# Performance work log

Hardware: AMD Instinct MI355X
Metric: run time of the kernel (lower is better)

Reference implementation:

```python
import jax, jax.numpy as jnp
import numpy as np

EPS = 1e-8

def setup_inputs() -> dict:
    key = jax.random.key(0)
    k1, k2, k3, k4, k5 = jax.random.split(key, 5)
    B, S, d, H = 4, 1024, 512, 8
    hd = d // H
    x = jax.random.normal(k1, (B, S, d), dtype=jnp.float32)
    V = jax.random.normal(k2, (B, S, H, hd), dtype=jnp.float32)
    # binary biological mask [B, S, S]
    M = (jax.random.uniform(k3, (B, S, S)) > 0.5).astype(jnp.float32)
    in_proj_w = jax.random.normal(k4, (3 * d, d), dtype=jnp.float32) * 0.02
    in_proj_b = jnp.zeros((3 * d,), dtype=jnp.float32)
    out_w = jax.random.normal(k5, (d, d), dtype=jnp.float32) * 0.02
    out_b = jnp.zeros((d,), dtype=jnp.float32)
    return {"x": x, "V": V, "M": M, "in_proj_w": in_proj_w,
            "in_proj_b": in_proj_b, "out_w": out_w, "out_b": out_b}


def reference(x, V, M, in_proj_w, in_proj_b, out_w, out_b):
    B, S, d = x.shape
    H, hd = V.shape[2], V.shape[3]
    # packed QKV projection (torch MHA in_proj); V slice is computed by torch
    # but its result is discarded, so only Q,K slices influence the output.
    qkv = x @ in_proj_w.T + in_proj_b            # [B, S, 3d]
    q = qkv[..., :d].reshape(B, S, H, hd).transpose(0, 2, 1, 3)        # [B,H,S,hd]
    k = qkv[..., d:2 * d].reshape(B, S, H, hd).transpose(0, 2, 1, 3)   # [B,H,S,hd]
    scores = jnp.einsum("bhqd,bhkd->bhqk", q, k) / jnp.sqrt(jnp.float32(hd))
    A = jax.nn.softmax(scores, axis=-1)           # [B,H,S,S] per-head attn weights
    # biological mask + L1 renormalization (post-hoc, as in original)
    A_sparse = A * M[:, None, :, :]
    norm = jnp.sum(jnp.abs(A_sparse), axis=-1, keepdims=True) + EPS
    A_bar = A_sparse / norm
    # custom V: [B,S,H,hd] -> [B,H,S,hd]
    Vp = V.transpose(0, 2, 1, 3)
    out = jnp.einsum("bhqk,bhkd->bhqd", A_bar, Vp)  # [B,H,S,hd]
    out = out.transpose(0, 2, 1, 3).reshape(B, S, d)
    return out @ out_w.T + out_b
```

## Files before the change

kernel.cpp:

```cpp
#include <hip/hip_runtime.h>
#include <hip/hip_bf16.h>

#define BB 4
#define SS 1024
#define DD 512
#define HH 8
#define HD 64

typedef __attribute__((ext_vector_type(8))) short bf16x8;
typedef __attribute__((ext_vector_type(4))) float f32x4;

static __device__ __forceinline__ unsigned short f2b(float f) {
  union { float f; unsigned int u; } c; c.f = f;
  return (unsigned short)((c.u + 0x7fffu + ((c.u >> 16) & 1u)) >> 16);
}

__global__ __launch_bounds__(256) void prep(
    const float* __restrict__ x, const float* __restrict__ W1,
    const float* __restrict__ Wo, const float* __restrict__ Mmask,
    const float* __restrict__ V, unsigned short* __restrict__ xb,
    unsigned short* __restrict__ W1b, unsigned short* __restrict__ Wob,
    unsigned char* __restrict__ Mpack, unsigned short* __restrict__ Vt) {
  __shared__ float Ls[64][65];
  const int bid = blockIdx.x;
  const int tid = threadIdx.x;

  if (bid < 1408) {
    const float* src; unsigned short* dst; size_t off;
    if (bid < 1024) { src = x;  dst = xb;  off = ((size_t)bid * 256 + tid) * 8; }
    else if (bid < 1280) { src = W1; dst = W1b; off = ((size_t)(bid - 1024) * 256 + tid) * 8; }
    else { src = Wo; dst = Wob; off = ((size_t)(bid - 1280) * 256 + tid) * 8; }
    const float4 a = *(const float4*)(src + off);
    const float4 b = *(const float4*)(src + off + 4);
    union { unsigned short s[8]; uint4 v; } o;
    o.s[0] = f2b(a.x); o.s[1] = f2b(a.y); o.s[2] = f2b(a.z); o.s[3] = f2b(a.w);
    o.s[4] = f2b(b.x); o.s[5] = f2b(b.y); o.s[6] = f2b(b.z); o.s[7] = f2b(b.w);
    *(uint4*)(dst + off) = o.v;
  } else if (bid < 3456) {
    const size_t g = (size_t)(bid - 1408) * 256 + tid;
    const float4 a = *(const float4*)(Mmask + g * 8);
    const float4 b = *(const float4*)(Mmask + g * 8 + 4);
    unsigned v = 0;
    v |= (a.x > 0.5f) ? 1u : 0u;   v |= (a.y > 0.5f) ? 2u : 0u;
    v |= (a.z > 0.5f) ? 4u : 0u;   v |= (a.w > 0.5f) ? 8u : 0u;
    v |= (b.x > 0.5f) ? 16u : 0u;  v |= (b.y > 0.5f) ? 32u : 0u;
    v |= (b.z > 0.5f) ? 64u : 0u;  v |= (b.w > 0.5f) ? 128u : 0u;
    Mpack[g] = (unsigned char)v;
  } else {
    const int id = bid - 3456;
    const int s0 = (id & 15) * 64, h = (id >> 4) & 7, b = id >> 7;
    {
      const int r = tid >> 2, cs = (tid & 3) * 16;
      const float* src = V + ((size_t)((b * SS + s0 + r) * HH) + h) * HD + cs;
#pragma unroll
      for (int j = 0; j < 4; j++) {
        const float4 v = *(const float4*)(src + j * 4);
        Ls[r][cs + j * 4 + 0] = v.x; Ls[r][cs + j * 4 + 1] = v.y;
        Ls[r][cs + j * 4 + 2] = v.z; Ls[r][cs + j * 4 + 3] = v.w;
      }
    }
    __syncthreads();
    {
      const int d = tid >> 2, ss = (tid & 3) * 16;
      union { unsigned short s[16]; uint4 v[2]; } o;
#pragma unroll
      for (int j = 0; j < 16; j++) o.s[j] = f2b(Ls[ss + j][d]);
      unsigned short* dst =
          Vt + ((size_t)((b * HH + h) * HD + d)) * SS + s0 + ss;
      *(uint4*)dst = o.v[0];
      *(uint4*)(dst + 8) = o.v[1];
    }
  }
}

__global__ __launch_bounds__(256) void gemm_qk(
    const unsigned short* __restrict__ xb, const unsigned short* __restrict__ W1b,
    const float* __restrict__ bias, unsigned short* __restrict__ qkb) {
  __shared__ unsigned short As[128][40];
  __shared__ unsigned short Bs[64][40];
  const int tid = threadIdx.x;
  const int lane = tid & 63, wave = tid >> 6;
  const int l16 = lane & 15, quad = lane >> 4;
  const int row0 = blockIdx.y * 128, col0 = blockIdx.x * 64;

  f32x4 acc[2][4];
#pragma unroll
  for (int i = 0; i < 2; i++)
#pragma unroll
    for (int j = 0; j < 4; j++) acc[i][j] = (f32x4){0.f, 0.f, 0.f, 0.f};

  for (int k0 = 0; k0 < DD; k0 += 32) {
    __syncthreads();
    {
      const int r = tid >> 1, cs = (tid & 1) * 16;
      const unsigned short* s = xb + (size_t)(row0 + r) * DD + k0 + cs;
      *(uint4*)&As[r][cs] = *(const uint4*)s;
      *(uint4*)&As[r][cs + 8] = *(const uint4*)(s + 8);
    }
    {
      const int r = tid >> 2, cs = (tid & 3) * 8;
      *(uint4*)&Bs[r][cs] =
          *(const uint4*)(W1b + (size_t)(col0 + r) * DD + k0 + cs);
    }
    __syncthreads();

    const bf16x8 a0 = *(const bf16x8*)&As[wave * 32 + l16][quad * 8];
    const bf16x8 a1 = *(const bf16x8*)&As[wave * 32 + 16 + l16][quad * 8];
#pragma unroll
    for (int nt = 0; nt < 4; nt++) {
      const bf16x8 bb = *(const bf16x8*)&Bs[nt * 16 + l16][quad * 8];
      acc[0][nt] = __builtin_amdgcn_mfma_f32_16x16x32_bf16(a0, bb, acc[0][nt], 0, 0, 0);
      acc[1][nt] = __builtin_amdgcn_mfma_f32_16x16x32_bf16(a1, bb, acc[1][nt], 0, 0, 0);
    }
  }

#pragma unroll
  for (int nt = 0; nt < 4; nt++) {
    const int col = col0 + nt * 16 + l16;
    const float bv = bias[col];
#pragma unroll
    for (int mi = 0; mi < 2; mi++)
#pragma unroll
      for (int reg = 0; reg < 4; reg++) {
        const int row = row0 + wave * 32 + mi * 16 + quad * 4 + reg;
        qkb[(size_t)row * 1024 + col] = f2b(acc[mi][nt][reg] + bv);
      }
  }
}

__global__ __launch_bounds__(256) void gemm_out(
    const unsigned short* __restrict__ Ab, const unsigned short* __restrict__ Wob,
    const float* __restrict__ bias, float* __restrict__ out) {
  __shared__ unsigned short As[64][40];
  __shared__ unsigned short Bs[64][40];
  const int tid = threadIdx.x;
  const int lane = tid & 63, wave = tid >> 6;
  const int l16 = lane & 15, quad = lane >> 4;
  const int row0 = blockIdx.y * 64, col0 = blockIdx.x * 64;

  f32x4 acc[4];
#pragma unroll
  for (int j = 0; j < 4; j++) acc[j] = (f32x4){0.f, 0.f, 0.f, 0.f};

  for (int k0 = 0; k0 < DD; k0 += 32) {
    __syncthreads();
    {
      const int r = tid >> 2, cs = (tid & 3) * 8;
      *(uint4*)&As[r][cs] =
          *(const uint4*)(Ab + (size_t)(row0 + r) * DD + k0 + cs);
      *(uint4*)&Bs[r][cs] =
          *(const uint4*)(Wob + (size_t)(col0 + r) * DD + k0 + cs);
    }
    __syncthreads();

    const bf16x8 a0 = *(const bf16x8*)&As[wave * 16 + l16][quad * 8];
#pragma unroll
    for (int nt = 0; nt < 4; nt++) {
      const bf16x8 bb = *(const bf16x8*)&Bs[nt * 16 + l16][quad * 8];
      acc[nt] = __builtin_amdgcn_mfma_f32_16x16x32_bf16(a0, bb, acc[nt], 0, 0, 0);
    }
  }

#pragma unroll
  for (int nt = 0; nt < 4; nt++) {
    const int col = col0 + nt * 16 + l16;
    const float bv = bias[col];
#pragma unroll
    for (int reg = 0; reg < 4; reg++) {
      const int row = row0 + wave * 16 + quad * 4 + reg;
      out[(size_t)row * DD + col] = acc[nt][reg] + bv;
    }
  }
}

__global__ __launch_bounds__(256) void flash_attn_split(
    const unsigned short* __restrict__ qkb, const unsigned short* __restrict__ Vt,
    const unsigned char* __restrict__ Mpack, float* __restrict__ Opart,
    float* __restrict__ Sms) {
  __shared__ unsigned short QP[64][72];
  __shared__ unsigned short Ks[64][72];
  __shared__ unsigned short Vs[64][72];

  const int tid = threadIdx.x;
  const int lane = tid & 63, wave = tid >> 6;
  const int l16 = lane & 15, quad = lane >> 4;
  const int q0 = blockIdx.x * 64;
  const int h = blockIdx.y & 7, sp = blockIdx.y >> 3;
  const int b = blockIdx.z;

  {
    const int r = tid >> 2, cs = (tid & 3) * 16;
    const unsigned short* s = qkb + (size_t)(b * SS + q0 + r) * 1024 + h * HD + cs;
    *(uint4*)&QP[r][cs] = *(const uint4*)s;
    *(uint4*)&QP[r][cs + 8] = *(const uint4*)(s + 8);
  }

  union { uint4 v[4]; unsigned w[16]; } mu;
  {
    const uint4* mp = (const uint4*)(Mpack +
        (size_t)(b * SS + q0 + wave * 16 + l16) * 128 + sp * 64);
    mu.v[0] = mp[0]; mu.v[1] = mp[1]; mu.v[2] = mp[2]; mu.v[3] = mp[3];
  }

  __syncthreads();
  const bf16x8 bQ0 = *(const bf16x8*)&QP[wave * 16 + l16][quad * 8];
  const bf16x8 bQ1 = *(const bf16x8*)&QP[wave * 16 + l16][32 + quad * 8];
  unsigned short(*Ps)[72] = (unsigned short(*)[72]) & QP[wave * 16][0];

  float Smp = 0.f;
  f32x4 O[4];
#pragma unroll
  for (int i = 0; i < 4; i++) O[i] = (f32x4){0.f, 0.f, 0.f, 0.f};

#pragma unroll
  for (int i = 0; i < 8; i++) {
    const int k0 = (sp * 8 + i) * 64;
    const unsigned mlo = mu.w[2 * i], mhi = mu.w[2 * i + 1];

    __syncthreads();
    {
      const int r = tid >> 2, cs = (tid & 3) * 16;
      const unsigned short* s =
          qkb + (size_t)(b * SS + k0 + r) * 1024 + DD + h * HD + cs;
      *(uint4*)&Ks[r][cs] = *(const uint4*)s;
      *(uint4*)&Ks[r][cs + 8] = *(const uint4*)(s + 8);
    }
    {
      const int d = tid >> 2, cs = (tid & 3) * 16;
      const unsigned short* s =
          Vt + ((size_t)((b * HH + h) * HD + d)) * SS + k0 + cs;
      *(uint4*)&Vs[d][cs] = *(const uint4*)s;
      *(uint4*)&Vs[d][cs + 8] = *(const uint4*)(s + 8);
    }
    __syncthreads();

#pragma unroll
    for (int t = 0; t < 4; t++) {
      const bf16x8 aK0 = *(const bf16x8*)&Ks[t * 16 + l16][quad * 8];
      const bf16x8 aK1 = *(const bf16x8*)&Ks[t * 16 + l16][32 + quad * 8];
      f32x4 a = (f32x4){0.f, 0.f, 0.f, 0.f};
      a = __builtin_amdgcn_mfma_f32_16x16x32_bf16(aK0, bQ0, a, 0, 0, 0);
      a = __builtin_amdgcn_mfma_f32_16x16x32_bf16(aK1, bQ1, a, 0, 0, 0);
      const unsigned nib =
          ((t < 2 ? mlo : mhi) >> ((t & 1) * 16 + quad * 4)) & 0xFu;
      float e0 = __expf(a[0] * 0.125f); e0 = (nib & 1u) ? e0 : 0.f;
      float e1 = __expf(a[1] * 0.125f); e1 = (nib & 2u) ? e1 : 0.f;
      float e2 = __expf(a[2] * 0.125f); e2 = (nib & 4u) ? e2 : 0.f;
      float e3 = __expf(a[3] * 0.125f); e3 = (nib & 8u) ? e3 : 0.f;
      Smp += (e0 + e1) + (e2 + e3);
      uint2 w;
      w.x = (unsigned)f2b(e0) | ((unsigned)f2b(e1) << 16);
      w.y = (unsigned)f2b(e2) | ((unsigned)f2b(e3) << 16);
      *(uint2*)&Ps[l16][t * 16 + quad * 4] = w;
    }

    const bf16x8 aP0 = *(const bf16x8*)&Ps[l16][quad * 8];
    const bf16x8 aP1 = *(const bf16x8*)&Ps[l16][32 + quad * 8];
#pragma unroll
    for (int dt = 0; dt < 4; dt++) {
      const bf16x8 bV0 = *(const bf16x8*)&Vs[dt * 16 + l16][quad * 8];
      const bf16x8 bV1 = *(const bf16x8*)&Vs[dt * 16 + l16][32 + quad * 8];
      O[dt] = __builtin_amdgcn_mfma_f32_16x16x32_bf16(aP0, bV0, O[dt], 0, 0, 0);
      O[dt] = __builtin_amdgcn_mfma_f32_16x16x32_bf16(aP1, bV1, O[dt], 0, 0, 0);
    }
  }

  Smp += __shfl_xor(Smp, 16);
  Smp += __shfl_xor(Smp, 32);
  const size_t grow0 = (size_t)(b * HH + h) * SS + q0 + wave * 16;
  const int NR = BB * HH * SS;
  if (lane < 16) Sms[(size_t)sp * NR + grow0 + lane] = Smp;
#pragma unroll
  for (int reg = 0; reg < 4; reg++) {
    const size_t obase = ((size_t)sp * NR + grow0 + quad * 4 + reg) * HD;
#pragma unroll
    for (int dt = 0; dt < 4; dt++)
      Opart[obase + dt * 16 + l16] = O[dt][reg];
  }
}

__global__ __launch_bounds__(256) void combine(
    const float* __restrict__ Opart, const float* __restrict__ Sms,
    unsigned short* __restrict__ attnb) {
  const int idx = blockIdx.x * 256 + threadIdx.x;
  const int row = idx >> 4;
  const int d = (idx & 15) * 4;
  const int NR = BB * HH * SS;
  const float4 o0 = *(const float4*)(Opart + (size_t)row * HD + d);
  const float4 o1 = *(const float4*)(Opart + ((size_t)NR + row) * HD + d);
  const float s = Sms[row] + Sms[NR + row];
  const float inv = 1.0f / (s + 1e-12f);
  const int b = row >> 13, h = (row >> 10) & 7, q = row & 1023;
  union { unsigned short us[4]; uint2 v; } o;
  o.us[0] = f2b((o0.x + o1.x) * inv);
  o.us[1] = f2b((o0.y + o1.y) * inv);
  o.us[2] = f2b((o0.z + o1.z) * inv);
  o.us[3] = f2b((o0.w + o1.w) * inv);
  *(uint2*)(attnb + (size_t)(b * SS + q) * DD + h * HD + d) = o.v;
}

extern "C" void kernel_launch(void* const* d_in, const int* in_sizes, int n_in,
                              void* d_out, int out_size, void* d_ws,
                              size_t ws_size, hipStream_t stream) {
  const float* x = (const float*)d_in[0];
  const float* V = (const float*)d_in[1];
  const float* Mmask = (const float*)d_in[2];
  const float* in_proj_w = (const float*)d_in[3];
  const float* in_proj_b = (const float*)d_in[4];
  const float* out_w = (const float*)d_in[5];
  const float* out_b = (const float*)d_in[6];
  float* out = (float*)d_out;

  unsigned char* ws = (unsigned char*)d_ws;
  unsigned short* qkb   = (unsigned short*)(ws);
  unsigned short* xb    = (unsigned short*)(ws + (8ull << 20));
  unsigned short* W1b   = (unsigned short*)(ws + (12ull << 20));
  unsigned short* Wob   = (unsigned short*)(ws + (13ull << 20));
  unsigned short* Vt    = (unsigned short*)(ws + (14ull << 20));
  unsigned short* attnb = (unsigned short*)(ws + (18ull << 20));
  float*          Opart = (float*)(ws + (22ull << 20));
  float*          Sms   = (float*)(ws + (38ull << 20));
  unsigned char*  Mpack = ws + (38ull << 20) + (256u << 10);

  prep<<<3968, 256, 0, stream>>>(x, in_proj_w, out_w, Mmask, V,
                                 xb, W1b, Wob, Mpack, Vt);
  gemm_qk<<<dim3(16, 32), 256, 0, stream>>>(xb, W1b, in_proj_b, qkb);
  flash_attn_split<<<dim3(SS / 64, 2 * HH, BB), 256, 0, stream>>>(
      qkb, Vt, Mpack, Opart, Sms);
  combine<<<2048, 256, 0, stream>>>(Opart, Sms, attnb);
  gemm_out<<<dim3(8, 64), 256, 0, stream>>>(attnb, Wob, out_b, out);
}
```

Before: 144.2 us.

## Register-prefetch next K tiles in GEMMs and attention, fold softmax scale into Q

Each of the three kernels (QK projection GEMM, output GEMM, split flash attention) now loads the next k-tile from global memory into registers right after the LDS barrier. Those loads overlap with the MFMA work on the current tile instead of stalling before it. The 1/sqrt(hd) scale moves from the attention exp into the Q-projection epilogue, so Q is stored pre-scaled in bf16 and the per-element multiply is dropped. This costs extra registers per thread and slightly changes bf16 rounding of Q.

After: 135.7 us. -5.9%, faster.

```diff
diff --git a/kernel.cpp b/kernel.cpp
--- a/kernel.cpp
+++ b/kernel.cpp
@@ -89,20 +89,25 @@
 #pragma unroll
     for (int j = 0; j < 4; j++) acc[i][j] = (f32x4){0.f, 0.f, 0.f, 0.f};
 
+  const int ra = tid >> 1, csa = (tid & 1) * 16;
+  const int rb = tid >> 2, csb = (tid & 3) * 8;
+  const unsigned short* ap = xb + (size_t)(row0 + ra) * DD + csa;
+  const unsigned short* bp = W1b + (size_t)(col0 + rb) * DD + csb;
+
+  uint4 pa0 = *(const uint4*)ap, pa1 = *(const uint4*)(ap + 8);
+  uint4 pb = *(const uint4*)bp;
+
   for (int k0 = 0; k0 < DD; k0 += 32) {
     __syncthreads();
-    {
-      const int r = tid >> 1, cs = (tid & 1) * 16;
-      const unsigned short* s = xb + (size_t)(row0 + r) * DD + k0 + cs;
-      *(uint4*)&As[r][cs] = *(const uint4*)s;
-      *(uint4*)&As[r][cs + 8] = *(const uint4*)(s + 8);
-    }
-    {
-      const int r = tid >> 2, cs = (tid & 3) * 8;
-      *(uint4*)&Bs[r][cs] =
-          *(const uint4*)(W1b + (size_t)(col0 + r) * DD + k0 + cs);
-    }
-    __syncthreads();
+    *(uint4*)&As[ra][csa] = pa0;
+    *(uint4*)&As[ra][csa + 8] = pa1;
+    *(uint4*)&Bs[rb][csb] = pb;
+    __syncthreads();
+    if (k0 + 32 < DD) {
+      pa0 = *(const uint4*)(ap + k0 + 32);
+      pa1 = *(const uint4*)(ap + k0 + 40);
+      pb = *(const uint4*)(bp + k0 + 32);
+    }
 
     const bf16x8 a0 = *(const bf16x8*)&As[wave * 32 + l16][quad * 8];
     const bf16x8 a1 = *(const bf16x8*)&As[wave * 32 + 16 + l16][quad * 8];
@@ -118,12 +123,13 @@
   for (int nt = 0; nt < 4; nt++) {
     const int col = col0 + nt * 16 + l16;
     const float bv = bias[col];
+    const float scale = (col < DD) ? 0.125f : 1.0f;
 #pragma unroll
     for (int mi = 0; mi < 2; mi++)
 #pragma unroll
       for (int reg = 0; reg < 4; reg++) {
         const int row = row0 + wave * 32 + mi * 16 + quad * 4 + reg;
-        qkb[(size_t)row * 1024 + col] = f2b(acc[mi][nt][reg] + bv);
+        qkb[(size_t)row * 1024 + col] = f2b((acc[mi][nt][reg] + bv) * scale);
       }
   }
 }
@@ -142,16 +148,22 @@
 #pragma unroll
   for (int j = 0; j < 4; j++) acc[j] = (f32x4){0.f, 0.f, 0.f, 0.f};
 
+  const int r = tid >> 2, cs = (tid & 3) * 8;
+  const unsigned short* ap = Ab + (size_t)(row0 + r) * DD + cs;
+  const unsigned short* bp = Wob + (size_t)(col0 + r) * DD + cs;
+
+  uint4 pa = *(const uint4*)ap;
+  uint4 pb = *(const uint4*)bp;
+
   for (int k0 = 0; k0 < DD; k0 += 32) {
     __syncthreads();
-    {
-      const int r = tid >> 2, cs = (tid & 3) * 8;
-      *(uint4*)&As[r][cs] =
-          *(const uint4*)(Ab + (size_t)(row0 + r) * DD + k0 + cs);
-      *(uint4*)&Bs[r][cs] =
-          *(const uint4*)(Wob + (size_t)(col0 + r) * DD + k0 + cs);
-    }
-    __syncthreads();
+    *(uint4*)&As[r][cs] = pa;
+    *(uint4*)&Bs[r][cs] = pb;
+    __syncthreads();
+    if (k0 + 32 < DD) {
+      pa = *(const uint4*)(ap + k0 + 32);
+      pb = *(const uint4*)(bp + k0 + 32);
+    }
 
     const bf16x8 a0 = *(const bf16x8*)&As[wave * 16 + l16][quad * 8];
 #pragma unroll
@@ -188,8 +200,9 @@
   const int h = blockIdx.y & 7, sp = blockIdx.y >> 3;
   const int b = blockIdx.z;
 
+  const int r = tid >> 2, cs = (tid & 3) * 16;
+
   {
-    const int r = tid >> 2, cs = (tid & 3) * 16;
     const unsigned short* s = qkb + (size_t)(b * SS + q0 + r) * 1024 + h * HD + cs;
     *(uint4*)&QP[r][cs] = *(const uint4*)s;
     *(uint4*)&QP[r][cs + 8] = *(const uint4*)(s + 8);
@@ -212,27 +225,31 @@
 #pragma unroll
   for (int i = 0; i < 4; i++) O[i] = (f32x4){0.f, 0.f, 0.f, 0.f};
 
+  const unsigned short* kp =
+      qkb + (size_t)(b * SS + sp * 8 * 64 + r) * 1024 + DD + h * HD + cs;
+  const unsigned short* vp =
+      Vt + ((size_t)((b * HH + h) * HD + r)) * SS + sp * 8 * 64 + cs;
+
+  uint4 pk0 = *(const uint4*)kp, pk1 = *(const uint4*)(kp + 8);
+  uint4 pv0 = *(const uint4*)vp, pv1 = *(const uint4*)(vp + 8);
+
 #pragma unroll
   for (int i = 0; i < 8; i++) {
-    const int k0 = (sp * 8 + i) * 64;
     const unsigned mlo = mu.w[2 * i], mhi = mu.w[2 * i + 1];
 
     __syncthreads();
-    {
-      const int r = tid >> 2, cs = (tid & 3) * 16;
-      const unsigned short* s =
-          qkb + (size_t)(b * SS + k0 + r) * 1024 + DD + h * HD + cs;
-      *(uint4*)&Ks[r][cs] = *(const uint4*)s;
-      *(uint4*)&Ks[r][cs + 8] = *(const uint4*)(s + 8);
-    }
-    {
-      const int d = tid >> 2, cs = (tid & 3) * 16;
-      const unsigned short* s =
-          Vt + ((size_t)((b * HH + h) * HD + d)) * SS + k0 + cs;
-      *(uint4*)&Vs[d][cs] = *(const uint4*)s;
-      *(uint4*)&Vs[d][cs + 8] = *(const uint4*)(s + 8);
-    }
-    __syncthreads();
+    *(uint4*)&Ks[r][cs] = pk0;
+    *(uint4*)&Ks[r][cs + 8] = pk1;
+    *(uint4*)&Vs[r][cs] = pv0;
+    *(uint4*)&Vs[r][cs + 8] = pv1;
+    __syncthreads();
+
+    if (i < 7) {
+      const unsigned short* nk = kp + (size_t)(i + 1) * 64 * 1024;
+      const unsigned short* nv = vp + (i + 1) * 64;
+      pk0 = *(const uint4*)nk; pk1 = *(const uint4*)(nk + 8);
+      pv0 = *(const uint4*)nv; pv1 = *(const uint4*)(nv + 8);
+    }
 
 #pragma unroll
     for (int t = 0; t < 4; t++) {
@@ -243,10 +260,10 @@
       a = __builtin_amdgcn_mfma_f32_16x16x32_bf16(aK1, bQ1, a, 0, 0, 0);
       const unsigned nib =
           ((t < 2 ? mlo : mhi) >> ((t & 1) * 16 + quad * 4)) & 0xFu;
-      float e0 = __expf(a[0] * 0.125f); e0 = (nib & 1u) ? e0 : 0.f;
-      float e1 = __expf(a[1] * 0.125f); e1 = (nib & 2u) ? e1 : 0.f;
-      float e2 = __expf(a[2] * 0.125f); e2 = (nib & 4u) ? e2 : 0.f;
-      float e3 = __expf(a[3] * 0.125f); e3 = (nib & 8u) ? e3 : 0.f;
+      float e0 = __expf(a[0]); e0 = (nib & 1u) ? e0 : 0.f;
+      float e1 = __expf(a[1]); e1 = (nib & 2u) ? e1 : 0.f;
+      float e2 = __expf(a[2]); e2 = (nib & 4u) ? e2 : 0.f;
+      float e3 = __expf(a[3]); e3 = (nib & 8u) ? e3 : 0.f;
       Smp += (e0 + e1) + (e2 + e3);
       uint2 w;
       w.x = (unsigned)f2b(e0) | ((unsigned)f2b(e1) << 16);
```
